# Kernel optimization log

Measured on AMD Instinct MI355X. Metric: run time of the kernel, lower is better.

Reference implementation:

```python
import jax, jax.numpy as jnp
import numpy as np
from jax import lax


def ternary_quantize(w):
    # alpha = mean(|w|); threshold = 0.7*alpha; map to {-1,0,1}*alpha
    alpha = jnp.mean(jnp.abs(w))
    threshold = 0.7 * alpha
    w_ternary = jnp.where(jnp.abs(w) < threshold, jnp.zeros_like(w), jnp.sign(w))
    return alpha * w_ternary


def setup_inputs() -> dict:
    key = jax.random.key(0)
    k1, k2 = jax.random.split(key)
    B, L, Cin = 32, 8192, 1
    K, F = 16, 256
    x = jax.random.normal(k1, (B, L, Cin), dtype=jnp.float32)
    # matches keras RandomUniform(-0.1, 0.1) initializer
    w = jax.random.uniform(k2, (K, Cin, F), dtype=jnp.float32, minval=-0.1, maxval=0.1)
    b = jnp.zeros((F,), dtype=jnp.float32)
    return {"x": x, "w": w, "b": b}


def reference(x, w, b):
    # x: (B, L, Cin) NWC; w: (K, Cin, F) WIO; stride 1, padding SAME
    w_q = ternary_quantize(w)
    y = lax.conv_general_dilated(
        x, w_q,
        window_strides=(1,),
        padding="SAME",
        dimension_numbers=("NWC", "WIO", "NWC"),
    )
    return y + b
```

## Files before the change

kernel.cpp:

```cpp
#include <hip/hip_runtime.h>
#include <hip/hip_bf16.h>

typedef float f32x4 __attribute__((ext_vector_type(4)));

__global__ __launch_bounds__(1024) void ternary_quant_kernel(
    const float* __restrict__ w, float* __restrict__ wq, int n) {
    __shared__ float red[1024];
    __shared__ float alpha_s;
    const int tid = threadIdx.x;
    float s = 0.f;
    for (int i = tid; i < n; i += 1024) s += fabsf(w[i]);
    red[tid] = s;
    __syncthreads();
    for (int off = 512; off > 0; off >>= 1) {
        if (tid < off) red[tid] += red[tid + off];
        __syncthreads();
    }
    if (tid == 0) alpha_s = red[0] / (float)n;
    __syncthreads();
    const float alpha = alpha_s;
    const float thr = 0.7f * alpha;
    for (int i = tid; i < n; i += 1024) {
        float v = w[i];
        float t = (fabsf(v) < thr) ? 0.f : (v > 0.f ? 1.f : (v < 0.f ? -1.f : 0.f));
        wq[i] = alpha * t;
    }
}

__global__ __launch_bounds__(256) void ternary_conv1d_kernel(
    const float* __restrict__ x,
    const float* __restrict__ wq,
    const float* __restrict__ bias,
    float* __restrict__ y,
    int L, int ltiles) {
    const int t  = threadIdx.x;
    const int fg = t & 63;
    const int ls = t >> 6;
    const int bid = blockIdx.x;
    const int lt = bid % ltiles;
    const int b  = bid / ltiles;
    const int l0 = lt * 64;

    __shared__ float xs[80];
    if (t < 79) {
        int gl = l0 - 7 + t;
        xs[t] = (gl >= 0 && gl < L) ? x[(size_t)b * L + gl] : 0.f;
    }

    f32x4 wv[16];
#pragma unroll
    for (int k = 0; k < 16; ++k)
        wv[k] = *reinterpret_cast<const f32x4*>(wq + k * 256 + fg * 4);
    const f32x4 bv = *reinterpret_cast<const f32x4*>(bias + fg * 4);

    __syncthreads();

    float xw[16];
#pragma unroll
    for (int j = 0; j < 16; ++j) xw[j] = xs[ls + j];

    f32x4* outp = reinterpret_cast<f32x4*>(y) + ((size_t)b * L + l0 + ls) * 64 + fg;
#pragma unroll
    for (int i = 0; i < 16; ++i) {
        f32x4 acc = bv;
#pragma unroll
        for (int k = 0; k < 16; ++k) {
            acc += wv[k] * xw[k];
        }
        *outp = acc;
        outp += 256;
        if (i < 15) {
#pragma unroll
            for (int j = 0; j < 12; ++j) xw[j] = xw[j + 4];
#pragma unroll
            for (int j = 12; j < 16; ++j) xw[j] = xs[ls + 4 * (i + 1) + j];
        }
    }
}

extern "C" void kernel_launch(void* const* d_in, const int* in_sizes, int n_in,
                              void* d_out, int out_size, void* d_ws, size_t ws_size,
                              hipStream_t stream) {
    const float* x = (const float*)d_in[0];
    const float* w = (const float*)d_in[1];
    const float* b = (const float*)d_in[2];
    float* y = (float*)d_out;
    float* wq = (float*)d_ws;

    const int B = 32;
    const int L = in_sizes[0] / B;
    const int nW = in_sizes[1];
    const int ltiles = L / 64;

    ternary_quant_kernel<<<1, 1024, 0, stream>>>(w, wq, nW);
    ternary_conv1d_kernel<<<B * ltiles, 256, 0, stream>>>(x, wq, b, y, L, ltiles);
}
```

Before: 51.77 us.

## Fuse ternary quantization into conv kernel and process four L-tiles per block

Removes the separate single-block quantization kernel: each conv block now recomputes the mean-abs reduction over all 4096 weights and quantizes its own slice in registers. Each block also loops over four 64-position tiles, so the grid shrinks to 1024 blocks and the redundant reduction is amortized. This removes a kernel launch and a serialized tiny kernel, at the cost of repeated reduction work per block and hardcoded sizes (4096 weights, L split into 32 groups of 256).

```diff
diff --git a/kernel.cpp b/kernel.cpp
--- a/kernel.cpp
+++ b/kernel.cpp
@@ -3,77 +3,82 @@
 
 typedef float f32x4 __attribute__((ext_vector_type(4)));
 
-__global__ __launch_bounds__(1024) void ternary_quant_kernel(
-    const float* __restrict__ w, float* __restrict__ wq, int n) {
-    __shared__ float red[1024];
-    __shared__ float alpha_s;
-    const int tid = threadIdx.x;
-    float s = 0.f;
-    for (int i = tid; i < n; i += 1024) s += fabsf(w[i]);
-    red[tid] = s;
-    __syncthreads();
-    for (int off = 512; off > 0; off >>= 1) {
-        if (tid < off) red[tid] += red[tid + off];
-        __syncthreads();
-    }
-    if (tid == 0) alpha_s = red[0] / (float)n;
-    __syncthreads();
-    const float alpha = alpha_s;
-    const float thr = 0.7f * alpha;
-    for (int i = tid; i < n; i += 1024) {
-        float v = w[i];
-        float t = (fabsf(v) < thr) ? 0.f : (v > 0.f ? 1.f : (v < 0.f ? -1.f : 0.f));
-        wq[i] = alpha * t;
-    }
-}
-
-__global__ __launch_bounds__(256) void ternary_conv1d_kernel(
+__global__ __launch_bounds__(256) void ternary_conv1d_fused(
     const float* __restrict__ x,
-    const float* __restrict__ wq,
+    const float* __restrict__ w,
     const float* __restrict__ bias,
     float* __restrict__ y,
-    int L, int ltiles) {
+    int L) {
     const int t  = threadIdx.x;
     const int fg = t & 63;
     const int ls = t >> 6;
     const int bid = blockIdx.x;
-    const int lt = bid % ltiles;
-    const int b  = bid / ltiles;
-    const int l0 = lt * 64;
+    const int b  = bid >> 5;
+    const int g  = bid & 31;
+    const int lbase = g * 256;
 
+    __shared__ float red[256];
     __shared__ float xs[80];
-    if (t < 79) {
-        int gl = l0 - 7 + t;
-        xs[t] = (gl >= 0 && gl < L) ? x[(size_t)b * L + gl] : 0.f;
+    __shared__ float alpha_s;
+
+    float s = 0.f;
+#pragma unroll
+    for (int j = 0; j < 16; ++j) s += fabsf(w[t + 256 * j]);
+    red[t] = s;
+    __syncthreads();
+    for (int off = 128; off > 0; off >>= 1) {
+        if (t < off) red[t] += red[t + off];
+        __syncthreads();
     }
+    if (t == 0) alpha_s = red[0] * (1.0f / 4096.0f);
+    __syncthreads();
+    const float alpha = alpha_s;
+    const float thr = 0.7f * alpha;
 
     f32x4 wv[16];
 #pragma unroll
-    for (int k = 0; k < 16; ++k)
-        wv[k] = *reinterpret_cast<const f32x4*>(wq + k * 256 + fg * 4);
+    for (int k = 0; k < 16; ++k) {
+        f32x4 v = *reinterpret_cast<const f32x4*>(w + k * 256 + fg * 4);
+        f32x4 q;
+#pragma unroll
+        for (int c = 0; c < 4; ++c) {
+            float vc = v[c];
+            float tc = (fabsf(vc) < thr) ? 0.f : (vc > 0.f ? 1.f : (vc < 0.f ? -1.f : 0.f));
+            q[c] = alpha * tc;
+        }
+        wv[k] = q;
+    }
     const f32x4 bv = *reinterpret_cast<const f32x4*>(bias + fg * 4);
 
-    __syncthreads();
+    for (int tt = 0; tt < 4; ++tt) {
+        const int l0 = lbase + tt * 64;
+        __syncthreads();
+        if (t < 79) {
+            int gl = l0 - 7 + t;
+            xs[t] = (gl >= 0 && gl < L) ? x[(size_t)b * L + gl] : 0.f;
+        }
+        __syncthreads();
 
-    float xw[16];
+        float xw[16];
 #pragma unroll
-    for (int j = 0; j < 16; ++j) xw[j] = xs[ls + j];
+        for (int j = 0; j < 16; ++j) xw[j] = xs[ls + j];
 
-    f32x4* outp = reinterpret_cast<f32x4*>(y) + ((size_t)b * L + l0 + ls) * 64 + fg;
+        f32x4* outp = reinterpret_cast<f32x4*>(y) + ((size_t)b * L + l0 + ls) * 64 + fg;
 #pragma unroll
-    for (int i = 0; i < 16; ++i) {
-        f32x4 acc = bv;
+        for (int i = 0; i < 16; ++i) {
+            f32x4 acc = bv;
 #pragma unroll
-        for (int k = 0; k < 16; ++k) {
-            acc += wv[k] * xw[k];
-        }
-        *outp = acc;
-        outp += 256;
-        if (i < 15) {
+            for (int k = 0; k < 16; ++k) {
+                acc += wv[k] * xw[k];
+            }
+            *outp = acc;
+            outp += 256;
+            if (i < 15) {
 #pragma unroll
-            for (int j = 0; j < 12; ++j) xw[j] = xw[j + 4];
+                for (int j = 0; j < 12; ++j) xw[j] = xw[j + 4];
 #pragma unroll
-            for (int j = 12; j < 16; ++j) xw[j] = xs[ls + 4 * (i + 1) + j];
+                for (int j = 12; j < 16; ++j) xw[j] = xs[ls + 4 * (i + 1) + j];
+            }
         }
     }
 }
@@ -85,13 +90,9 @@
     const float* w = (const float*)d_in[1];
     const float* b = (const float*)d_in[2];
     float* y = (float*)d_out;
-    float* wq = (float*)d_ws;
 
     const int B = 32;
     const int L = in_sizes[0] / B;
-    const int nW = in_sizes[1];
-    const int ltiles = L / 64;
 
-    ternary_quant_kernel<<<1, 1024, 0, stream>>>(w, wq, nW);
-    ternary_conv1d_kernel<<<B * ltiles, 256, 0, stream>>>(x, wq, b, y, L, ltiles);
+    ternary_conv1d_fused<<<B * 32, 256, 0, stream>>>(x, w, b, y, L);
 }
```

Result: no change. 51.63 us (-0.3%).
